# Kernel optimization log

Hardware: AMD Instinct MI355X
Metric: run time of the kernel (lower is better)

## Reference

```python
import jax, jax.numpy as jnp
import numpy as np

B, T, C, H = 8, 1024, 512, 8


def setup_inputs() -> dict:
    key = jax.random.key(0)
    k1, k2, k3, k4 = jax.random.split(key, 4)
    x = jax.random.normal(k1, (B, T, C), jnp.float32)
    q = jax.random.normal(k2, (B, T, C), jnp.float32)
    W_kv = jax.random.normal(k3, (C, 2 * C), jnp.float32) * 0.02
    W_proj = jax.random.normal(k4, (C, C), jnp.float32) * 0.02
    return {"x": x, "q": q, "W_kv": W_kv, "W_proj": W_proj}


def reference(x, q, W_kv, W_proj):
    B, T, C = x.shape
    H = 8
    D = C // H
    T2 = T // 2
    # kv projection (nn.Linear, no bias)
    kv = x @ W_kv                      # [B,T,2C]
    k, v = kv[..., :C], kv[..., C:]
    # 7 batch-dim rolls of the first half, then reinterpret [7,B,T2,C] -> [B,7*T2,C]
    # (exactly what torch.stack(...).view(B,-1,C) does on the contiguous buffer)
    sk = jnp.stack([jnp.roll(k[:, :T2], i, axis=0) for i in range(7)]).reshape(B, -1, C)
    sv = jnp.stack([jnp.roll(v[:, :T2], i, axis=0) for i in range(7)]).reshape(B, -1, C)
    k = jnp.concatenate((sk, k), axis=1)   # [B, S, C], S = 7*T2 + T
    v = jnp.concatenate((sv, v), axis=1)
    qh = q.reshape(B, T, H, D).transpose(0, 2, 1, 3)    # [B,H,T,D]
    kh = k.reshape(B, -1, H, D).transpose(0, 2, 1, 3)   # [B,H,S,D]
    vh = v.reshape(B, -1, H, D).transpose(0, 2, 1, 3)   # [B,H,S,D]
    scale = 1.0 / jnp.sqrt(jnp.float32(D))
    # NOTE: the torch module passes attn_mask=None to SDPA, so attention is unmasked
    scores = jnp.einsum('bhld,bhsd->bhls', qh, kh) * scale
    attn = jax.nn.softmax(scores, axis=-1)
    y = jnp.einsum('bhls,bhsd->bhld', attn, vh)
    y = y.transpose(0, 2, 1, 3).reshape(B, T, C)
    return y @ W_proj
```

## Files before the change

kernel.cpp:

```cpp
#include <hip/hip_runtime.h>

typedef __bf16 bf16;
typedef bf16 bf16x8 __attribute__((ext_vector_type(8)));
typedef bf16 bf16x4 __attribute__((ext_vector_type(4)));
typedef float f32x4 __attribute__((ext_vector_type(4)));
typedef float f32x16 __attribute__((ext_vector_type(16)));
typedef unsigned int u32;

#define DEV_INLINE __device__ __forceinline__

DEV_INLINE f32x4 mfma16(bf16x8 a, bf16x8 b, f32x4 c) {
    return __builtin_amdgcn_mfma_f32_16x16x32_bf16(a, b, c, 0, 0, 0);
}
DEV_INLINE f32x16 mfma32(bf16x8 a, bf16x8 b, f32x16 c) {
    return __builtin_amdgcn_mfma_f32_32x32x16_bf16(a, b, c, 0, 0, 0);
}

#define GLD16(gp, lp) __builtin_amdgcn_global_load_lds( \
    (const __attribute__((address_space(1))) void*)(gp), \
    (__attribute__((address_space(3))) void*)(lp), 16, 0, 0)

__global__ void cast_scale_kernel(const float* __restrict__ in, bf16* __restrict__ out,
                                  float scale, int n4) {
    int i = blockIdx.x * blockDim.x + threadIdx.x;
    if (i < n4) {
        f32x4 v = reinterpret_cast<const f32x4*>(in)[i];
        bf16x4 o;
        o[0] = (bf16)(v[0] * scale);
        o[1] = (bf16)(v[1] * scale);
        o[2] = (bf16)(v[2] * scale);
        o[3] = (bf16)(v[3] * scale);
        reinterpret_cast<bf16x4*>(out)[i] = o;
    }
}

__global__ void transpose_cast_kernel(const float* __restrict__ in, bf16* __restrict__ out,
                                      int K, int N) {
    int idx = blockIdx.x * blockDim.x + threadIdx.x;
    if (idx < K * N) {
        int n = idx / K, k = idx - n * K;
        out[idx] = (bf16)in[k * N + n];
    }
}

__launch_bounds__(256, 2)
__global__ void gemm_kv_kernel(const bf16* __restrict__ A,
                               const bf16* __restrict__ Bt,
                               bf16* __restrict__ Kout,
                               bf16* __restrict__ Vt)
{
    __shared__ bf16 As[128][32];
    __shared__ bf16 Bs[128][32];
    const int bm = blockIdx.x, bn = blockIdx.y;
    const int tid = threadIdx.x;
    const int lane = tid & 63, w = tid >> 6;
    const int wm = (w >> 1) * 64, wn = (w & 1) * 64;
    const int lr = lane & 15, kg = lane >> 4;

    const f32x4 fz = {0.f, 0.f, 0.f, 0.f};
    f32x4 acc[4][4];
    for (int i = 0; i < 4; ++i)
        for (int j = 0; j < 4; ++j) acc[i][j] = fz;

    const int srow = tid >> 2, sc4 = tid & 3;

    for (int k0 = 0; k0 < 512; k0 += 32) {
        __syncthreads();
        for (int rr = 0; rr < 2; ++rr) {
            int row = srow + rr * 64;
            *reinterpret_cast<bf16x8*>(&As[row][(sc4 ^ (row & 3)) << 3]) =
                *reinterpret_cast<const bf16x8*>(A + (size_t)(bm * 128 + row) * 512 + k0 + (sc4 << 3));
            *reinterpret_cast<bf16x8*>(&Bs[row][(sc4 ^ (row & 3)) << 3]) =
                *reinterpret_cast<const bf16x8*>(Bt + (size_t)(bn * 128 + row) * 512 + k0 + (sc4 << 3));
        }
        __syncthreads();
        bf16x8 af[4], bfr[4];
        for (int mi = 0; mi < 4; ++mi) {
            int row = wm + mi * 16 + lr;
            af[mi] = *reinterpret_cast<const bf16x8*>(&As[row][(kg ^ (row & 3)) << 3]);
        }
        for (int ni = 0; ni < 4; ++ni) {
            int row = wn + ni * 16 + lr;
            bfr[ni] = *reinterpret_cast<const bf16x8*>(&Bs[row][(kg ^ (row & 3)) << 3]);
        }
        for (int mi = 0; mi < 4; ++mi)
            for (int ni = 0; ni < 4; ++ni)
                acc[mi][ni] = mfma16(af[mi], bfr[ni], acc[mi][ni]);
    }

    for (int mi = 0; mi < 4; ++mi) {
        int mbase = bm * 128 + wm + mi * 16 + kg * 4;
        for (int ni = 0; ni < 4; ++ni) {
            int col = bn * 128 + wn + ni * 16 + lr;
            if (col < 512) {
                for (int r = 0; r < 4; ++r)
                    Kout[(size_t)(mbase + r) * 512 + col] = (bf16)acc[mi][ni][r];
            } else {
                int c = col - 512, h = c >> 6, d = c & 63;
                int b = mbase >> 10, t = mbase & 1023;
                int tp = (t & ~12) | ((t & 4) << 1) | ((t & 8) >> 1);
                bf16x4 pk;
                for (int r = 0; r < 4; ++r) pk[r] = (bf16)acc[mi][ni][r];
                *reinterpret_cast<bf16x4*>(Vt + (size_t)((b * 8 + h) * 64 + d) * 1024 + tp) = pk;
            }
        }
    }
}

__launch_bounds__(256, 2)
__global__ void gemm_proj_kernel(const bf16* __restrict__ A,
                                 const bf16* __restrict__ Bt,
                                 float* __restrict__ out)
{
    __shared__ bf16 As[128][32];
    __shared__ bf16 Bs[128][32];
    const int bm = blockIdx.x, bn = blockIdx.y;
    const int tid = threadIdx.x;
    const int lane = tid & 63, w = tid >> 6;
    const int wm = (w >> 1) * 64, wn = (w & 1) * 64;
    const int lr = lane & 15, kg = lane >> 4;

    const f32x4 fz = {0.f, 0.f, 0.f, 0.f};
    f32x4 acc[4][4];
    for (int i = 0; i < 4; ++i)
        for (int j = 0; j < 4; ++j) acc[i][j] = fz;

    const int srow = tid >> 2, sc4 = tid & 3;

    for (int k0 = 0; k0 < 512; k0 += 32) {
        __syncthreads();
        for (int rr = 0; rr < 2; ++rr) {
            int row = srow + rr * 64;
            *reinterpret_cast<bf16x8*>(&As[row][(sc4 ^ (row & 3)) << 3]) =
                *reinterpret_cast<const bf16x8*>(A + (size_t)(bm * 128 + row) * 512 + k0 + (sc4 << 3));
            *reinterpret_cast<bf16x8*>(&Bs[row][(sc4 ^ (row & 3)) << 3]) =
                *reinterpret_cast<const bf16x8*>(Bt + (size_t)(bn * 128 + row) * 512 + k0 + (sc4 << 3));
        }
        __syncthreads();
        bf16x8 af[4], bfr[4];
        for (int mi = 0; mi < 4; ++mi) {
            int row = wm + mi * 16 + lr;
            af[mi] = *reinterpret_cast<const bf16x8*>(&As[row][(kg ^ (row & 3)) << 3]);
        }
        for (int ni = 0; ni < 4; ++ni) {
            int row = wn + ni * 16 + lr;
            bfr[ni] = *reinterpret_cast<const bf16x8*>(&Bs[row][(kg ^ (row & 3)) << 3]);
        }
        for (int mi = 0; mi < 4; ++mi)
            for (int ni = 0; ni < 4; ++ni)
                acc[mi][ni] = mfma16(af[mi], bfr[ni], acc[mi][ni]);
    }

    for (int mi = 0; mi < 4; ++mi) {
        int mbase = bm * 128 + wm + mi * 16 + kg * 4;
        for (int ni = 0; ni < 4; ++ni) {
            int col = bn * 128 + wn + ni * 16 + lr;
            for (int r = 0; r < 4; ++r)
                out[(size_t)(mbase + r) * 512 + col] = acc[mi][ni][r];
        }
    }
}

__launch_bounds__(512, 2)
__global__ void attn_kernel(const bf16* __restrict__ Qb,
                            const bf16* __restrict__ Kb,
                            const bf16* __restrict__ Vt,
                            bf16* __restrict__ Y)
{
    __shared__ bf16 sK[2][128][64];
    __shared__ bf16 sV[2][64][128];

    const int raw = blockIdx.x;
    const int h = raw & 7;
    const int qseg = (raw >> 3) & 3;
    const int b = raw >> 5;
    const int tid = threadIdx.x, lane = tid & 63, w = tid >> 6;
    const int lq = lane & 31, hi = lane >> 5;
    const int qrow = b * 1024 + qseg * 256 + w * 32 + lq;

    bf16x8 qf[4];
#pragma unroll
    for (int ds = 0; ds < 4; ++ds)
        qf[ds] = *reinterpret_cast<const bf16x8*>(
            Qb + (size_t)qrow * 512 + h * 64 + ds * 16 + hi * 8);

    const f32x16 Z16 = {0,0,0,0,0,0,0,0,0,0,0,0,0,0,0,0};
    f32x16 O0 = Z16, O1 = Z16, lv = Z16;

    const bf16* Kf = &sK[0][0][0];
    const bf16* Vf = &sV[0][0][0];
    int koffE[4];
#pragma unroll
    for (int ds = 0; ds < 4; ++ds)
        koffE[ds] = lq * 64 + (((ds * 2 + hi) ^ (lq & 7)) * 8);
    int voffE[2][4];
#pragma unroll
    for (int half = 0; half < 2; ++half)
#pragma unroll
        for (int ssub = 0; ssub < 4; ++ssub)
            voffE[half][ssub] = lq * 128 + (((half * 8 + ssub * 2 + hi) ^ (lq & 15)) * 8);

    const int krow = w * 16 + (lane >> 3);
    const size_t koff = (size_t)krow * 512 + (((lane & 7) ^ ((lane >> 3) & 7)) * 8);
    const int vrowA = w * 8 + (lane >> 4);
    const int vrowB = vrowA + 4;
    const size_t voffA = (size_t)vrowA * 1024 + (((lane & 15) ^ (vrowA & 15)) * 8);
    const size_t voffB = (size_t)vrowB * 1024 + (((lane & 15) ^ (vrowB & 15)) * 8);

    auto kv_base = [&](int t, const bf16*& kp, const bf16*& vp) {
        int jj = t >> 2, st = t & 3;
        int src_b, tb;
        if (jj < 7) { int m7 = 7 * b + jj; src_b = ((m7 & 7) - (m7 >> 3)) & 7; tb = 0; }
        else        { src_b = b; tb = (jj - 7) * 512; }
        int tpos = tb + st * 128;
        kp = Kb + (size_t)(src_b * 1024 + tpos) * 512 + h * 64;
        vp = Vt + (size_t)((src_b * 8 + h) * 64) * 1024 + tpos;
    };

    auto stage = [&](int buf, int t) {
        const bf16 *kp, *vp;
        kv_base(t, kp, vp);
        GLD16(kp + koff,           &sK[buf][w * 16][0]);
        GLD16(kp + koff + 8 * 512, &sK[buf][w * 16 + 8][0]);
        GLD16(vp + voffA,          &sV[buf][w * 8][0]);
        GLD16(vp + voffB,          &sV[buf][w * 8 + 4][0]);
    };

    auto computeTile = [&](int cb) {
#pragma unroll
        for (int half = 0; half < 2; ++half) {
            const int kb = cb * 8192 + half * 4096;
            f32x16 s0, s1;
#pragma unroll
            for (int i = 0; i < 16; ++i) { s0[i] = -4.0f; s1[i] = -4.0f; }
            __builtin_amdgcn_s_setprio(1);
#pragma unroll
            for (int ds = 0; ds < 4; ++ds) {
                bf16x8 k0 = *reinterpret_cast<const bf16x8*>(Kf + kb + koffE[ds]);
                bf16x8 k1 = *reinterpret_cast<const bf16x8*>(Kf + kb + 2048 + koffE[ds]);
                s0 = mfma32(k0, qf[ds], s0);
                s1 = mfma32(k1, qf[ds], s1);
            }
            __builtin_amdgcn_s_setprio(0);

#pragma unroll
            for (int i = 0; i < 16; ++i) {
                float p0 = exp2f(s0[i]); s0[i] = p0;
                float p1 = exp2f(s1[i]); s1[i] = p1;
                lv[i] += p0 + p1;
            }

            __builtin_amdgcn_s_setprio(1);
#pragma unroll
            for (int ssub = 0; ssub < 4; ++ssub) {
                bf16x8 pf;
#pragma unroll
                for (int i = 0; i < 8; ++i) {
                    float pv = (ssub < 2) ? ((ssub & 1) ? s0[8 + i] : s0[i])
                                          : ((ssub & 1) ? s1[8 + i] : s1[i]);
                    pf[i] = (bf16)pv;
                }
                bf16x8 a0 = *reinterpret_cast<const bf16x8*>(Vf + cb * 8192 + voffE[half][ssub]);
                bf16x8 a1 = *reinterpret_cast<const bf16x8*>(Vf + cb * 8192 + 4096 + voffE[half][ssub]);
                O0 = mfma32(a0, pf, O0);
                O1 = mfma32(a1, pf, O1);
            }
            __builtin_amdgcn_s_setprio(0);
        }
    };

    stage(0, 0);

    for (int t = 0; t < 36; t += 2) {
        __syncthreads();
        stage(1, t + 1);
        computeTile(0);
        __syncthreads();
        if (t + 2 < 36) stage(0, t + 2);
        computeTile(1);
    }

    float lrun = 0.f;
#pragma unroll
    for (int i = 0; i < 16; ++i) lrun += lv[i];
    lrun += __shfl_xor(lrun, 32);
    const float inv = 1.0f / lrun;
#pragma unroll
    for (int dh = 0; dh < 2; ++dh) {
#pragma unroll
        for (int q4 = 0; q4 < 4; ++q4) {
            bf16x4 pk;
#pragma unroll
            for (int i = 0; i < 4; ++i) {
                float o = (dh ? O1[q4 * 4 + i] : O0[q4 * 4 + i]) * inv;
                pk[i] = (bf16)o;
            }
            *reinterpret_cast<bf16x4*>(
                Y + (size_t)qrow * 512 + h * 64 + dh * 32 + q4 * 8 + hi * 4) = pk;
        }
    }
}

extern "C" void kernel_launch(void* const* d_in, const int* in_sizes, int n_in,
                              void* d_out, int out_size, void* d_ws, size_t ws_size,
                              hipStream_t stream) {
    const float* x   = (const float*)d_in[0];
    const float* q   = (const float*)d_in[1];
    const float* Wkv = (const float*)d_in[2];
    const float* Wp  = (const float*)d_in[3];
    float* out = (float*)d_out;

    char* ws = (char*)d_ws;
    bf16* xb   = (bf16*)(ws);
    bf16* qb   = (bf16*)(ws + 8388608);
    bf16* Kb   = (bf16*)(ws + 16777216);
    bf16* Vt   = (bf16*)(ws + 25165824);
    bf16* Yb   = (bf16*)(ws + 33554432);
    bf16* Wkvt = (bf16*)(ws + 41943040);
    bf16* Wpt  = (bf16*)(ws + 42991616);

    const int n4 = 8192 * 512 / 4;
    cast_scale_kernel<<<n4 / 256, 256, 0, stream>>>(x, xb, 1.0f, n4);
    cast_scale_kernel<<<n4 / 256, 256, 0, stream>>>(q, qb, 0.18033688011112306f, n4);
    transpose_cast_kernel<<<(512 * 1024) / 256, 256, 0, stream>>>(Wkv, Wkvt, 512, 1024);
    transpose_cast_kernel<<<(512 * 512) / 256, 256, 0, stream>>>(Wp, Wpt, 512, 512);
    gemm_kv_kernel<<<dim3(64, 8), 256, 0, stream>>>(xb, Wkvt, Kb, Vt);
    attn_kernel<<<256, 512, 0, stream>>>(qb, Kb, Vt, Yb);
    gemm_proj_kernel<<<dim3(64, 4), 256, 0, stream>>>(Yb, Wpt, out);
}
```

Baseline: 157.5 us.

## Split attention over two KV halves and fuse input casts into consumers

New measurement: 159.4 us. Within noise of the previous version (+1.2%).

```diff
diff --git a/kernel.cpp b/kernel.cpp
--- a/kernel.cpp
+++ b/kernel.cpp
@@ -20,20 +20,6 @@
     (const __attribute__((address_space(1))) void*)(gp), \
     (__attribute__((address_space(3))) void*)(lp), 16, 0, 0)
 
-__global__ void cast_scale_kernel(const float* __restrict__ in, bf16* __restrict__ out,
-                                  float scale, int n4) {
-    int i = blockIdx.x * blockDim.x + threadIdx.x;
-    if (i < n4) {
-        f32x4 v = reinterpret_cast<const f32x4*>(in)[i];
-        bf16x4 o;
-        o[0] = (bf16)(v[0] * scale);
-        o[1] = (bf16)(v[1] * scale);
-        o[2] = (bf16)(v[2] * scale);
-        o[3] = (bf16)(v[3] * scale);
-        reinterpret_cast<bf16x4*>(out)[i] = o;
-    }
-}
-
 __global__ void transpose_cast_kernel(const float* __restrict__ in, bf16* __restrict__ out,
                                       int K, int N) {
     int idx = blockIdx.x * blockDim.x + threadIdx.x;
@@ -44,7 +30,7 @@
 }
 
 __launch_bounds__(256, 2)
-__global__ void gemm_kv_kernel(const bf16* __restrict__ A,
+__global__ void gemm_kv_kernel(const float* __restrict__ A,
                                const bf16* __restrict__ Bt,
                                bf16* __restrict__ Kout,
                                bf16* __restrict__ Vt)
@@ -68,8 +54,12 @@
         __syncthreads();
         for (int rr = 0; rr < 2; ++rr) {
             int row = srow + rr * 64;
-            *reinterpret_cast<bf16x8*>(&As[row][(sc4 ^ (row & 3)) << 3]) =
-                *reinterpret_cast<const bf16x8*>(A + (size_t)(bm * 128 + row) * 512 + k0 + (sc4 << 3));
+            const float* ap = A + (size_t)(bm * 128 + row) * 512 + k0 + (sc4 << 3);
+            f32x4 a0 = *reinterpret_cast<const f32x4*>(ap);
+            f32x4 a1 = *reinterpret_cast<const f32x4*>(ap + 4);
+            bf16x8 av;
+            for (int j = 0; j < 4; ++j) { av[j] = (bf16)a0[j]; av[4 + j] = (bf16)a1[j]; }
+            *reinterpret_cast<bf16x8*>(&As[row][(sc4 ^ (row & 3)) << 3]) = av;
             *reinterpret_cast<bf16x8*>(&Bs[row][(sc4 ^ (row & 3)) << 3]) =
                 *reinterpret_cast<const bf16x8*>(Bt + (size_t)(bn * 128 + row) * 512 + k0 + (sc4 << 3));
         }
@@ -162,27 +152,38 @@
 }
 
 __launch_bounds__(512, 2)
-__global__ void attn_kernel(const bf16* __restrict__ Qb,
+__global__ void attn_kernel(const float* __restrict__ Qr,
                             const bf16* __restrict__ Kb,
                             const bf16* __restrict__ Vt,
-                            bf16* __restrict__ Y)
+                            bf16* __restrict__ Op,
+                            float* __restrict__ Lp)
 {
     __shared__ bf16 sK[2][128][64];
     __shared__ bf16 sV[2][64][128];
 
     const int raw = blockIdx.x;
     const int h = raw & 7;
-    const int qseg = (raw >> 3) & 3;
-    const int b = raw >> 5;
+    const int shalf = (raw >> 3) & 1;
+    const int qseg = (raw >> 4) & 3;
+    const int b = raw >> 6;
     const int tid = threadIdx.x, lane = tid & 63, w = tid >> 6;
     const int lq = lane & 31, hi = lane >> 5;
     const int qrow = b * 1024 + qseg * 256 + w * 32 + lq;
-
+    const int tbase0 = shalf * 18;
+
+    const float QSC = 0.18033688011112306f;
     bf16x8 qf[4];
 #pragma unroll
-    for (int ds = 0; ds < 4; ++ds)
-        qf[ds] = *reinterpret_cast<const bf16x8*>(
-            Qb + (size_t)qrow * 512 + h * 64 + ds * 16 + hi * 8);
+    for (int ds = 0; ds < 4; ++ds) {
+        const float* qp = Qr + (size_t)qrow * 512 + h * 64 + ds * 16 + hi * 8;
+        f32x4 q0 = *reinterpret_cast<const f32x4*>(qp);
+        f32x4 q1 = *reinterpret_cast<const f32x4*>(qp + 4);
+#pragma unroll
+        for (int j = 0; j < 4; ++j) {
+            qf[ds][j]     = (bf16)(q0[j] * QSC);
+            qf[ds][4 + j] = (bf16)(q1[j] * QSC);
+        }
+    }
 
     const f32x16 Z16 = {0,0,0,0,0,0,0,0,0,0,0,0,0,0,0,0};
     f32x16 O0 = Z16, O1 = Z16, lv = Z16;
@@ -208,7 +209,8 @@
     const size_t voffB = (size_t)vrowB * 1024 + (((lane & 15) ^ (vrowB & 15)) * 8);
 
     auto kv_base = [&](int t, const bf16*& kp, const bf16*& vp) {
-        int jj = t >> 2, st = t & 3;
+        int gt = tbase0 + t;
+        int jj = gt >> 2, st = gt & 3;
         int src_b, tb;
         if (jj < 7) { int m7 = 7 * b + jj; src_b = ((m7 & 7) - (m7 >> 3)) & 7; tb = 0; }
         else        { src_b = b; tb = (jj - 7) * 512; }
@@ -271,12 +273,12 @@
 
     stage(0, 0);
 
-    for (int t = 0; t < 36; t += 2) {
+    for (int t = 0; t < 18; t += 2) {
         __syncthreads();
         stage(1, t + 1);
         computeTile(0);
         __syncthreads();
-        if (t + 2 < 36) stage(0, t + 2);
+        if (t + 2 < 18) stage(0, t + 2);
         computeTile(1);
     }
 
@@ -284,21 +286,39 @@
 #pragma unroll
     for (int i = 0; i < 16; ++i) lrun += lv[i];
     lrun += __shfl_xor(lrun, 32);
-    const float inv = 1.0f / lrun;
+    if (hi == 0) Lp[shalf * 65536 + h * 8192 + qrow] = lrun;
+
+    bf16* Od = Op + (size_t)shalf * 4194304;
 #pragma unroll
     for (int dh = 0; dh < 2; ++dh) {
 #pragma unroll
         for (int q4 = 0; q4 < 4; ++q4) {
             bf16x4 pk;
 #pragma unroll
-            for (int i = 0; i < 4; ++i) {
-                float o = (dh ? O1[q4 * 4 + i] : O0[q4 * 4 + i]) * inv;
-                pk[i] = (bf16)o;
-            }
+            for (int i = 0; i < 4; ++i)
+                pk[i] = (bf16)(dh ? O1[q4 * 4 + i] : O0[q4 * 4 + i]);
             *reinterpret_cast<bf16x4*>(
-                Y + (size_t)qrow * 512 + h * 64 + dh * 32 + q4 * 8 + hi * 4) = pk;
-        }
-    }
+                Od + (size_t)qrow * 512 + h * 64 + dh * 32 + q4 * 8 + hi * 4) = pk;
+        }
+    }
+}
+
+__global__ void combine_kernel(const bf16* __restrict__ Op, const float* __restrict__ Lp,
+                               bf16* __restrict__ Y) {
+    int i = blockIdx.x * blockDim.x + threadIdx.x;
+    int row = i >> 6;
+    int col8 = (i & 63) * 8;
+    int h = col8 >> 6;
+    float l = Lp[h * 8192 + row] + Lp[65536 + h * 8192 + row];
+    float inv = 1.0f / l;
+    size_t off = (size_t)row * 512 + col8;
+    bf16x8 a = *reinterpret_cast<const bf16x8*>(Op + off);
+    bf16x8 c = *reinterpret_cast<const bf16x8*>(Op + 4194304 + off);
+    bf16x8 o;
+#pragma unroll
+    for (int j = 0; j < 8; ++j)
+        o[j] = (bf16)(((float)a[j] + (float)c[j]) * inv);
+    *reinterpret_cast<bf16x8*>(Y + off) = o;
 }
 
 extern "C" void kernel_launch(void* const* d_in, const int* in_sizes, int n_in,
@@ -311,20 +331,18 @@
     float* out = (float*)d_out;
 
     char* ws = (char*)d_ws;
-    bf16* xb   = (bf16*)(ws);
-    bf16* qb   = (bf16*)(ws + 8388608);
-    bf16* Kb   = (bf16*)(ws + 16777216);
-    bf16* Vt   = (bf16*)(ws + 25165824);
-    bf16* Yb   = (bf16*)(ws + 33554432);
-    bf16* Wkvt = (bf16*)(ws + 41943040);
-    bf16* Wpt  = (bf16*)(ws + 42991616);
-
-    const int n4 = 8192 * 512 / 4;
-    cast_scale_kernel<<<n4 / 256, 256, 0, stream>>>(x, xb, 1.0f, n4);
-    cast_scale_kernel<<<n4 / 256, 256, 0, stream>>>(q, qb, 0.18033688011112306f, n4);
+    bf16*  Kb   = (bf16*)(ws);
+    bf16*  Vt   = (bf16*)(ws + 8388608);
+    bf16*  Opar = (bf16*)(ws + 16777216);
+    bf16*  Yb   = (bf16*)(ws + 33554432);
+    bf16*  Wkvt = (bf16*)(ws + 41943040);
+    bf16*  Wpt  = (bf16*)(ws + 42991616);
+    float* Lp   = (float*)(ws + 43515904);
+
     transpose_cast_kernel<<<(512 * 1024) / 256, 256, 0, stream>>>(Wkv, Wkvt, 512, 1024);
     transpose_cast_kernel<<<(512 * 512) / 256, 256, 0, stream>>>(Wp, Wpt, 512, 512);
-    gemm_kv_kernel<<<dim3(64, 8), 256, 0, stream>>>(xb, Wkvt, Kb, Vt);
-    attn_kernel<<<256, 512, 0, stream>>>(qb, Kb, Vt, Yb);
+    gemm_kv_kernel<<<dim3(64, 8), 256, 0, stream>>>(x, Wkvt, Kb, Vt);
+    attn_kernel<<<512, 512, 0, stream>>>(q, Kb, Vt, Opar, Lp);
+    combine_kernel<<<(8192 * 512 / 8) / 256, 256, 0, stream>>>(Opar, Lp, Yb);
     gemm_proj_kernel<<<dim3(64, 4), 256, 0, stream>>>(Yb, Wpt, out);
 }
```
